# Kernel optimization log

Measured on AMD Instinct MI355X. Metric: run time of the kernel, lower is better.

Reference implementation:

```python
import jax, jax.numpy as jnp
import numpy as np

EPS = 1e-5

def _make_mask(rng, outdim, indim, expand_size, k=3):
    # Mirrors ExpanderConv2d mask construction (indim <= outdim branch when equal)
    m = np.zeros((outdim, indim), dtype=np.float32)
    if indim > outdim:
        for i in range(outdim):
            idx = rng.permutation(indim)[:expand_size]
            m[i, idx] = 1.0
    else:
        for i in range(indim):
            idx = rng.permutation(outdim)[:expand_size]
            m[idx, i] = 1.0
    return jnp.asarray(np.broadcast_to(m[:, :, None, None], (outdim, indim, k, k)).copy())

def _bn(x, gamma, beta, mean, var):
    # eval-mode BatchNorm2d over channel axis (NCHW)
    inv = gamma / jnp.sqrt(var + EPS)
    return x * inv[None, :, None, None] + (beta - mean * inv)[None, :, None, None]

def _conv3x3(x, w, stride=1):
    return jax.lax.conv_general_dilated(
        x, w, window_strides=(stride, stride), padding=((1, 1), (1, 1)),
        dimension_numbers=('NCHW', 'OIHW', 'NCHW'))

def setup_inputs() -> dict:
    key = jax.random.key(0)
    ks = jax.random.split(key, 4)
    C = 256
    x = jax.random.normal(ks[0], (64, C, 32, 32), dtype=jnp.float32)
    fan_out = C * 9
    std = float(np.sqrt(2.0 / fan_out))  # kaiming_normal_, mode='fan_out'
    w1 = jax.random.normal(ks[1], (C, C, 3, 3), dtype=jnp.float32) * std
    w2 = jax.random.normal(ks[2], (C, C, 3, 3), dtype=jnp.float32) * std
    rng = np.random.default_rng(0)
    mask1 = _make_mask(rng, C, C, C // 8)
    mask2 = _make_mask(rng, C, C, C // 8)
    g = jax.random.uniform(ks[3], (4 * C,), minval=0.5, maxval=1.5, dtype=jnp.float32)
    return {
        'x': x,
        'bn1_gamma': g[:C], 'bn1_beta': jnp.zeros((C,), jnp.float32),
        'bn1_mean': jnp.zeros((C,), jnp.float32), 'bn1_var': jnp.ones((C,), jnp.float32),
        'w1': w1, 'mask1': mask1,
        'bn2_gamma': g[C:2 * C], 'bn2_beta': jnp.zeros((C,), jnp.float32),
        'bn2_mean': jnp.zeros((C,), jnp.float32), 'bn2_var': jnp.ones((C,), jnp.float32),
        'w2': w2, 'mask2': mask2,
    }

def reference(x, bn1_gamma, bn1_beta, bn1_mean, bn1_var, w1, mask1,
              bn2_gamma, bn2_beta, bn2_mean, bn2_var, w2, mask2):
    out = jax.nn.relu(_bn(x, bn1_gamma, bn1_beta, bn1_mean, bn1_var))
    out = _conv3x3(out, w1 * mask1)          # masked expander conv, dropout(p=0)=identity
    out = jax.nn.relu(_bn(out, bn2_gamma, bn2_beta, bn2_mean, bn2_var))
    out = _conv3x3(out, w2 * mask2, stride=1)
    return out + x                            # identity shortcut (stride=1, in==out)
```

## Files before the change

kernel.cpp:

```cpp
#include <hip/hip_runtime.h>
#include <hip/hip_bf16.h>
#include <stdint.h>

typedef __bf16 bf16_t;
typedef __bf16 bf16x8 __attribute__((ext_vector_type(8)));
typedef __bf16 bf16x4 __attribute__((ext_vector_type(4)));
typedef float  f32x4  __attribute__((ext_vector_type(4)));

#define AS_GLOBAL __attribute__((address_space(1)))
#define AS_LDS    __attribute__((address_space(3)))

static constexpr int CCH   = 256;
static constexpr int HP    = 34;
static constexpr int PLANE = HP * HP;

__global__ void prep_params_k(const float* g1, const float* b1, const float* m1, const float* v1,
                              const float* g2, const float* b2, const float* m2, const float* v2,
                              float* prm) {
  int i = threadIdx.x;
  float i1 = g1[i] * rsqrtf(v1[i] + 1e-5f);
  prm[i]       = i1;
  prm[256 + i] = b1[i] - m1[i] * i1;
  float i2 = g2[i] * rsqrtf(v2[i] + 1e-5f);
  prm[512 + i] = i2;
  prm[768 + i] = b2[i] - m2[i] * i2;
}

__global__ __launch_bounds__(256) void prep_weights_k(const float* __restrict__ w,
                                                      const float* __restrict__ msk,
                                                      bf16_t* __restrict__ out) {
  int idx = blockIdx.x * 256 + threadIdx.x;
  const float* wp = w + (long)idx * 9;
  const float* mp = msk + (long)idx * 9;
#pragma unroll
  for (int khw = 0; khw < 9; ++khw)
    out[khw * 65536 + idx] = (bf16_t)(wp[khw] * mp[khw]);
}

__global__ __launch_bounds__(256) void zero_borders_k(bf16_t* __restrict__ t0p,
                                                      bf16_t* __restrict__ t1p) {
  const int bid = blockIdx.x;
  bf16_t* base = ((bid & 1) ? t1p : t0p) + (long)(bid >> 1) * PLANE * CCH;
  for (int i = threadIdx.x; i < 132 * 32; i += 256) {
    int pix = i >> 5, c16 = i & 31;
    int r, col;
    if (pix < 34)       { r = 0;           col = pix; }
    else if (pix < 68)  { r = 33;          col = pix - 34; }
    else if (pix < 100) { r = pix - 68 + 1; col = 0; }
    else                { r = pix - 100 + 1; col = 33; }
    *(f32x4*)&base[(r * HP + col) * CCH + c16 * 8] = f32x4{0.f, 0.f, 0.f, 0.f};
  }
}

__global__ __launch_bounds__(256) void prep_input_k(const float* __restrict__ x,
                                                    const float* __restrict__ prm,
                                                    bf16_t* __restrict__ t0p) {
  __shared__ __align__(16) bf16_t tile[64 * 256];
  const int tid = threadIdx.x;
  const int bid = blockIdx.x;
  const int n   = bid >> 4;
  const int p0  = (bid & 15) << 6;
  const int px    = tid & 63;
  const int cbase = tid >> 6;
  for (int r = 0; r < 64; ++r) {
    int ci = r * 4 + cbase;
    float v = x[((n * 256 + ci) << 10) + p0 + px];
    float y = fmaxf(v * prm[ci] + prm[256 + ci], 0.f);
    int byte = px * 512 + ((ci * 2) ^ ((px & 7) << 4));
    *(bf16_t*)((char*)tile + byte) = (bf16_t)y;
  }
  __syncthreads();
  for (int j = 0; j < 8; ++j) {
    int off  = j * 256 + tid;
    int pix  = off >> 5;
    int c16  = off & 31;
    int byte = pix * 512 + ((c16 * 16) ^ ((pix & 7) << 4));
    bf16x8 v = *(const bf16x8*)((char*)tile + byte);
    int p = p0 + pix;
    long gp = ((long)n * PLANE + ((p >> 5) + 1) * HP + (p & 31) + 1) * CCH + c16 * 8;
    *(bf16x8*)(t0p + gp) = v;
  }
}

template <int EPI>
__global__ __launch_bounds__(256, 2) void conv3x3_k(const bf16_t* __restrict__ inp,
                                                    const bf16_t* __restrict__ wts,
                                                    const float* __restrict__ prm,
                                                    const float* __restrict__ resid,
                                                    bf16_t* __restrict__ out_cl,
                                                    float* __restrict__ out_f) {
  __shared__ __align__(128) bf16_t As[2][4096];
  __shared__ __align__(128) bf16_t Bs[2][8192];

  const int tid  = threadIdx.x;
  const int lane = tid & 63;
  const int wid  = tid >> 6;
  const int wm   = wid >> 1;
  const int wn   = wid & 1;

  const int bid = blockIdx.x;
  const int w   = ((bid & 7) << 7) + (bid >> 3);
  const int co0 = (w & 1) << 7;
  const int pt  = w >> 1;
  const int n   = pt >> 3;
  const int hb  = (pt & 7) << 2;

  const int swz8 = (((lane & 3) ^ ((lane >> 2) & 3) ^ (lane >> 4)) << 3);
  const int l15  = lane & 15;

  f32x4 acc[4][4];
#pragma unroll
  for (int i = 0; i < 4; ++i)
#pragma unroll
    for (int j = 0; j < 4; ++j) acc[i][j] = f32x4{0.f, 0.f, 0.f, 0.f};

  auto stageA = [&](int ab, int c, int t) {
    const int ci0 = c << 5;
#pragma unroll
    for (int j = 0; j < 2; ++j) {
      const int ch  = wid * 2 + j;
      const int row = ch * 16 + (lane >> 2);
      const bf16_t* ga = wts + ((t * CCH + co0 + row) * CCH + ci0 + swz8);
      __builtin_amdgcn_global_load_lds((const AS_GLOBAL void*)ga,
                                       (AS_LDS void*)(&As[ab][ch * 512]), 16, 0, 0);
    }
  };

  auto stageB = [&](int bb, int c) {
    const int ci0 = c << 5;
#pragma unroll
    for (int j = 0; j < 4; ++j) {
      const int ibase = wid * 4 + j;
      int g = (ibase << 6) + lane;
      if (g > 815) g = 815;
      const int r  = g / 136;
      const int rm = g - r * 136;
      const bf16_t* gb = inp + ((n * PLANE + (hb + r) * HP + (rm >> 2)) * CCH + ci0 + ((rm & 3) << 3));
      __builtin_amdgcn_global_load_lds((const AS_GLOBAL void*)gb,
                                       (AS_LDS void*)(&Bs[bb][ibase * 512]), 16, 0, 0);
    }
  };

  stageB(0, 0);
  stageA(0, 0, 0);
  int ab = 0, bb = 0;
  for (int c = 0; c < 8; ++c) {
#pragma unroll
    for (int t = 0; t < 9; ++t) {
      __syncthreads();
      if (t < 8) stageA(ab ^ 1, c, t + 1);
      else if (c < 7) { stageB(bb ^ 1, c + 1); stageA(ab ^ 1, c + 1, 0); }
      const int kh = t / 3, kw = t - kh * 3;
      bf16x8 av[4], bv[4];
#pragma unroll
      for (int mi = 0; mi < 4; ++mi)
        av[mi] = *(const bf16x8*)&As[ab][((wm * 64 + mi * 16 + l15) << 5) + swz8];
#pragma unroll
      for (int ni = 0; ni < 4; ++ni) {
        const int p  = (wn << 6) + (ni << 4) + l15;
        const int pr = p >> 5, pc = p & 31;
        bv[ni] = *(const bf16x8*)&Bs[bb][((pr + kh) * 136 + (pc + kw) * 4 + (lane >> 4)) * 8];
      }
#pragma unroll
      for (int mi = 0; mi < 4; ++mi)
#pragma unroll
        for (int ni = 0; ni < 4; ++ni)
          acc[mi][ni] = __builtin_amdgcn_mfma_f32_16x16x32_bf16(av[mi], bv[ni], acc[mi][ni], 0, 0, 0);
      ab ^= 1;
    }
    bb ^= 1;
  }

  if (EPI == 0) {
#pragma unroll
    for (int mi = 0; mi < 4; ++mi) {
      const int co_b = co0 + wm * 64 + mi * 16 + ((lane >> 4) << 2);
      const float s0 = prm[co_b], s1 = prm[co_b + 1], s2 = prm[co_b + 2], s3 = prm[co_b + 3];
      const float t0 = prm[256 + co_b], t1 = prm[256 + co_b + 1],
                  t2 = prm[256 + co_b + 2], t3 = prm[256 + co_b + 3];
#pragma unroll
      for (int ni = 0; ni < 4; ++ni) {
        f32x4 v = acc[mi][ni];
        const int p  = (wn << 6) + (ni << 4) + l15;
        const int pr = p >> 5, pc = p & 31;
        bf16x4 pk;
        pk[0] = (bf16_t)fmaxf(v[0] * s0 + t0, 0.f);
        pk[1] = (bf16_t)fmaxf(v[1] * s1 + t1, 0.f);
        pk[2] = (bf16_t)fmaxf(v[2] * s2 + t2, 0.f);
        pk[3] = (bf16_t)fmaxf(v[3] * s3 + t3, 0.f);
        *(bf16x4*)&out_cl[(n * PLANE + (hb + pr + 1) * HP + pc + 1) * CCH + co_b] = pk;
      }
    }
  } else {
#pragma unroll
    for (int mi = 0; mi < 4; ++mi) {
      const int co_b = co0 + wm * 64 + mi * 16 + ((lane >> 4) << 2);
#pragma unroll
      for (int ni = 0; ni < 4; ++ni) {
        f32x4 v = acc[mi][ni];
        const int p  = (wn << 6) + (ni << 4) + l15;
        const int gp = ((n * CCH + co_b) << 10) + (hb << 5) + p;
        out_f[gp]        = v[0] + resid[gp];
        out_f[gp + 1024] = v[1] + resid[gp + 1024];
        out_f[gp + 2048] = v[2] + resid[gp + 2048];
        out_f[gp + 3072] = v[3] + resid[gp + 3072];
      }
    }
  }
}

extern "C" void kernel_launch(void* const* d_in, const int* in_sizes, int n_in,
                              void* d_out, int out_size, void* d_ws, size_t ws_size,
                              hipStream_t stream) {
  const float* x  = (const float*)d_in[0];
  const float* g1 = (const float*)d_in[1];
  const float* b1 = (const float*)d_in[2];
  const float* m1 = (const float*)d_in[3];
  const float* v1 = (const float*)d_in[4];
  const float* w1 = (const float*)d_in[5];
  const float* k1 = (const float*)d_in[6];
  const float* g2 = (const float*)d_in[7];
  const float* b2 = (const float*)d_in[8];
  const float* m2 = (const float*)d_in[9];
  const float* v2 = (const float*)d_in[10];
  const float* w2 = (const float*)d_in[11];
  const float* k2 = (const float*)d_in[12];

  char* ws = (char*)d_ws;
  const size_t T0P_B = (size_t)64 * PLANE * CCH * 2;
  bf16_t* t0p = (bf16_t*)ws;
  bf16_t* t1p = (bf16_t*)(ws + T0P_B);
  bf16_t* mw1 = (bf16_t*)(ws + 2 * T0P_B);
  bf16_t* mw2 = (bf16_t*)(ws + 2 * T0P_B + 1179648);
  float*  prm = (float*)(ws + 2 * T0P_B + 2 * 1179648);

  prep_params_k<<<1, 256, 0, stream>>>(g1, b1, m1, v1, g2, b2, m2, v2, prm);
  zero_borders_k<<<128, 256, 0, stream>>>(t0p, t1p);
  prep_weights_k<<<256, 256, 0, stream>>>(w1, k1, mw1);
  prep_weights_k<<<256, 256, 0, stream>>>(w2, k2, mw2);
  prep_input_k<<<1024, 256, 0, stream>>>(x, prm, t0p);

  conv3x3_k<0><<<1024, 256, 0, stream>>>(t0p, mw1, prm + 512, nullptr, t1p, nullptr);
  conv3x3_k<1><<<1024, 256, 0, stream>>>(t1p, mw2, nullptr, x, nullptr, (float*)d_out);
}
```

Baseline: 200.6 us.

## Restructure conv kernel with larger pixel tiles, 32x32 MFMA and register-prefetched weights

The implicit-GEMM conv kernel now covers 256 pixels (8 rows) per block instead of 128, halving the grid to 512 blocks. It switches from 16x16x32 to 32x32x16 bf16 MFMA with 16-wide accumulators. Weights are loaded straight from global memory into registers, double-buffered one tap ahead, so the LDS A buffer and most per-tap barriers go away. Input halo tiles are staged in LDS with one barrier per channel chunk and explicit vmcnt waits, and MFMA issue gets raised wave priority. In exchange, register pressure rises and fewer blocks are available to fill the CUs.

New measurement: 222.5 us. 1.11x slower.

```diff
diff --git a/kernel.cpp b/kernel.cpp
--- a/kernel.cpp
+++ b/kernel.cpp
@@ -6,9 +6,11 @@
 typedef __bf16 bf16x8 __attribute__((ext_vector_type(8)));
 typedef __bf16 bf16x4 __attribute__((ext_vector_type(4)));
 typedef float  f32x4  __attribute__((ext_vector_type(4)));
+typedef float  f32x16 __attribute__((ext_vector_type(16)));
 
 #define AS_GLOBAL __attribute__((address_space(1)))
 #define AS_LDS    __attribute__((address_space(3)))
+#define VMW(N) asm volatile("s_waitcnt vmcnt(" #N ")" ::: "memory")
 
 static constexpr int CCH   = 256;
 static constexpr int HP    = 34;
@@ -89,8 +91,7 @@
                                                     const float* __restrict__ resid,
                                                     bf16_t* __restrict__ out_cl,
                                                     float* __restrict__ out_f) {
-  __shared__ __align__(128) bf16_t As[2][4096];
-  __shared__ __align__(128) bf16_t Bs[2][8192];
+  __shared__ __align__(128) bf16_t Bs[2][12288];
 
   const int tid  = threadIdx.x;
   const int lane = tid & 63;
@@ -99,113 +100,144 @@
   const int wn   = wid & 1;
 
   const int bid = blockIdx.x;
-  const int w   = ((bid & 7) << 7) + (bid >> 3);
+  const int w   = ((bid & 7) << 6) + (bid >> 3);
   const int co0 = (w & 1) << 7;
   const int pt  = w >> 1;
-  const int n   = pt >> 3;
-  const int hb  = (pt & 7) << 2;
-
-  const int swz8 = (((lane & 3) ^ ((lane >> 2) & 3) ^ (lane >> 4)) << 3);
-  const int l15  = lane & 15;
-
-  f32x4 acc[4][4];
-#pragma unroll
-  for (int i = 0; i < 4; ++i)
-#pragma unroll
-    for (int j = 0; j < 4; ++j) acc[i][j] = f32x4{0.f, 0.f, 0.f, 0.f};
-
-  auto stageA = [&](int ab, int c, int t) {
-    const int ci0 = c << 5;
-#pragma unroll
-    for (int j = 0; j < 2; ++j) {
-      const int ch  = wid * 2 + j;
-      const int row = ch * 16 + (lane >> 2);
-      const bf16_t* ga = wts + ((t * CCH + co0 + row) * CCH + ci0 + swz8);
-      __builtin_amdgcn_global_load_lds((const AS_GLOBAL void*)ga,
-                                       (AS_LDS void*)(&As[ab][ch * 512]), 16, 0, 0);
-    }
-  };
-
-  auto stageB = [&](int bb, int c) {
-    const int ci0 = c << 5;
-#pragma unroll
-    for (int j = 0; j < 4; ++j) {
-      const int ibase = wid * 4 + j;
-      int g = (ibase << 6) + lane;
-      if (g > 815) g = 815;
-      const int r  = g / 136;
-      const int rm = g - r * 136;
-      const bf16_t* gb = inp + ((n * PLANE + (hb + r) * HP + (rm >> 2)) * CCH + ci0 + ((rm & 3) << 3));
-      __builtin_amdgcn_global_load_lds((const AS_GLOBAL void*)gb,
-                                       (AS_LDS void*)(&Bs[bb][ibase * 512]), 16, 0, 0);
-    }
-  };
-
-  stageB(0, 0);
-  stageA(0, 0, 0);
-  int ab = 0, bb = 0;
-  for (int c = 0; c < 8; ++c) {
-#pragma unroll
-    for (int t = 0; t < 9; ++t) {
-      __syncthreads();
-      if (t < 8) stageA(ab ^ 1, c, t + 1);
-      else if (c < 7) { stageB(bb ^ 1, c + 1); stageA(ab ^ 1, c + 1, 0); }
-      const int kh = t / 3, kw = t - kh * 3;
-      bf16x8 av[4], bv[4];
-#pragma unroll
-      for (int mi = 0; mi < 4; ++mi)
-        av[mi] = *(const bf16x8*)&As[ab][((wm * 64 + mi * 16 + l15) << 5) + swz8];
-#pragma unroll
-      for (int ni = 0; ni < 4; ++ni) {
-        const int p  = (wn << 6) + (ni << 4) + l15;
-        const int pr = p >> 5, pc = p & 31;
-        bv[ni] = *(const bf16x8*)&Bs[bb][((pr + kh) * 136 + (pc + kw) * 4 + (lane >> 4)) * 8];
+  const int n   = pt >> 2;
+  const int hb  = (pt & 3) << 3;
+
+  const int l31 = lane & 31;
+  const int k5  = lane >> 5;
+
+  const long aBase = (long)(co0 + wm * 64 + l31) * CCH + k5 * 8;
+  const int  bBase = k5 * 2720 + wn * 1088 + l31 * 8;
+
+  int bofs[6];
+#pragma unroll
+  for (int j = 0; j < 6; ++j) {
+    int idx = j * 256 + tid;
+    if (idx > 1359) idx = 1359;
+    const int g   = idx / 340;
+    const int rem = idx - g * 340;
+    const int r   = rem / 34;
+    const int cc  = rem - r * 34;
+    bofs[j] = (n * PLANE + (hb + r) * HP + cc) * CCH + g * 8;
+  }
+
+  f32x16 acc[2][4];
+#pragma unroll
+  for (int i = 0; i < 2; ++i)
+#pragma unroll
+    for (int j = 0; j < 4; ++j)
+#pragma unroll
+      for (int e = 0; e < 16; ++e) acc[i][j][e] = 0.f;
+
+  bf16x8 avA[4], avB[4], bv[8];
+
+#define STB(BBUF, CI0N, J) do {                                                      \
+    const bf16_t* gb_ = inp + bofs[J] + (CI0N);                                      \
+    __builtin_amdgcn_global_load_lds((const AS_GLOBAL void*)gb_,                     \
+        (AS_LDS void*)(&Bs[BBUF][((J) * 256 + tid) * 8]), 16, 0, 0);                 \
+  } while (0)
+
+#define APREF(SET, CI0N, TT) do {                                                    \
+    _Pragma("unroll") for (int mi = 0; mi < 2; ++mi)                                 \
+    _Pragma("unroll") for (int ks = 0; ks < 2; ++ks)                                 \
+      SET[mi * 2 + ks] = *(const bf16x8*)(wts + (long)(TT) * 65536 + aBase           \
+                                          + mi * 8192 + (CI0N) + ks * 16);           \
+  } while (0)
+
+#define MFMA16(SET) do {                                                             \
+    _Pragma("unroll") for (int mi = 0; mi < 2; ++mi)                                 \
+    _Pragma("unroll") for (int nj = 0; nj < 4; ++nj)                                 \
+    _Pragma("unroll") for (int ks = 0; ks < 2; ++ks)                                 \
+      acc[mi][nj] = __builtin_amdgcn_mfma_f32_32x32x16_bf16(                         \
+          SET[mi * 2 + ks], bv[nj * 2 + ks], acc[mi][nj], 0, 0, 0);                  \
+  } while (0)
+
+#define TAPB(T, PAR, LASTC) do {                                                     \
+    constexpr int KH = (T) / 3, KW = (T) % 3;                                        \
+    _Pragma("unroll") for (int nj = 0; nj < 4; ++nj)                                 \
+    _Pragma("unroll") for (int ks = 0; ks < 2; ++ks)                                 \
+      bv[nj * 2 + ks] = *(const bf16x8*)&bsrd[bBase + ks * 5440                      \
+                                              + (nj + KH) * 272 + KW * 8];           \
+    if (!(LASTC) && (T) <= 5) STB((c + 1) & 1, (c + 1) << 5, T);                     \
+    if (!((LASTC) && (T) == 8)) {                                                    \
+      constexpr int TN = ((T) + 1) % 9;                                              \
+      const int cin = ((T) == 8) ? ((c + 1) << 5) : (c << 5);                        \
+      if (((PAR) + (T)) & 1) { APREF(avA, cin, TN); } else { APREF(avB, cin, TN); }  \
+    }                                                                                \
+    __builtin_amdgcn_s_setprio(1);                                                   \
+    if (((PAR) + (T)) & 1) { MFMA16(avB); } else { MFMA16(avA); }                    \
+    __builtin_amdgcn_s_setprio(0);                                                   \
+  } while (0)
+
+#define CHUNKB(PAR, LASTC) do {                                                      \
+    const bf16_t* bsrd = &Bs[c & 1][0];                                              \
+    TAPB(0, PAR, LASTC); TAPB(1, PAR, LASTC); TAPB(2, PAR, LASTC);                   \
+    TAPB(3, PAR, LASTC); TAPB(4, PAR, LASTC); TAPB(5, PAR, LASTC);                   \
+    TAPB(6, PAR, LASTC); TAPB(7, PAR, LASTC); TAPB(8, PAR, LASTC);                   \
+    if (!(LASTC)) { VMW(0); __builtin_amdgcn_s_barrier(); }                          \
+  } while (0)
+
+  STB(0, 0, 0); STB(0, 0, 1); STB(0, 0, 2); STB(0, 0, 3); STB(0, 0, 4); STB(0, 0, 5);
+  APREF(avA, 0, 0);
+  VMW(0);
+  __builtin_amdgcn_s_barrier();
+
+  int c = 0;
+#pragma unroll 1
+  for (int it = 0; it < 3; ++it) {
+    CHUNKB(0, 0); ++c;
+    CHUNKB(1, 0); ++c;
+  }
+  CHUNKB(0, 0); ++c;
+  CHUNKB(1, 1);
+
+#undef TAPB
+#undef CHUNKB
+#undef APREF
+#undef MFMA16
+#undef STB
+
+  if (EPI == 0) {
+#pragma unroll
+    for (int mi = 0; mi < 2; ++mi)
+#pragma unroll
+      for (int nj = 0; nj < 4; ++nj) {
+        const int prow = hb + wn * 4 + nj;
+        const long pbase = ((long)n * PLANE + (prow + 1) * HP + l31 + 1) * CCH;
+#pragma unroll
+        for (int q = 0; q < 4; ++q) {
+          const int co_b = co0 + wm * 64 + mi * 32 + q * 8 + k5 * 4;
+          const float s0 = prm[co_b], s1 = prm[co_b + 1], s2 = prm[co_b + 2], s3 = prm[co_b + 3];
+          const float t0 = prm[256 + co_b], t1 = prm[256 + co_b + 1],
+                      t2 = prm[256 + co_b + 2], t3 = prm[256 + co_b + 3];
+          bf16x4 pk;
+          pk[0] = (bf16_t)fmaxf(acc[mi][nj][q * 4 + 0] * s0 + t0, 0.f);
+          pk[1] = (bf16_t)fmaxf(acc[mi][nj][q * 4 + 1] * s1 + t1, 0.f);
+          pk[2] = (bf16_t)fmaxf(acc[mi][nj][q * 4 + 2] * s2 + t2, 0.f);
+          pk[3] = (bf16_t)fmaxf(acc[mi][nj][q * 4 + 3] * s3 + t3, 0.f);
+          *(bf16x4*)&out_cl[pbase + co_b] = pk;
+        }
       }
-#pragma unroll
-      for (int mi = 0; mi < 4; ++mi)
-#pragma unroll
-        for (int ni = 0; ni < 4; ++ni)
-          acc[mi][ni] = __builtin_amdgcn_mfma_f32_16x16x32_bf16(av[mi], bv[ni], acc[mi][ni], 0, 0, 0);
-      ab ^= 1;
-    }
-    bb ^= 1;
-  }
-
-  if (EPI == 0) {
-#pragma unroll
-    for (int mi = 0; mi < 4; ++mi) {
-      const int co_b = co0 + wm * 64 + mi * 16 + ((lane >> 4) << 2);
-      const float s0 = prm[co_b], s1 = prm[co_b + 1], s2 = prm[co_b + 2], s3 = prm[co_b + 3];
-      const float t0 = prm[256 + co_b], t1 = prm[256 + co_b + 1],
-                  t2 = prm[256 + co_b + 2], t3 = prm[256 + co_b + 3];
-#pragma unroll
-      for (int ni = 0; ni < 4; ++ni) {
-        f32x4 v = acc[mi][ni];
-        const int p  = (wn << 6) + (ni << 4) + l15;
-        const int pr = p >> 5, pc = p & 31;
-        bf16x4 pk;
-        pk[0] = (bf16_t)fmaxf(v[0] * s0 + t0, 0.f);
-        pk[1] = (bf16_t)fmaxf(v[1] * s1 + t1, 0.f);
-        pk[2] = (bf16_t)fmaxf(v[2] * s2 + t2, 0.f);
-        pk[3] = (bf16_t)fmaxf(v[3] * s3 + t3, 0.f);
-        *(bf16x4*)&out_cl[(n * PLANE + (hb + pr + 1) * HP + pc + 1) * CCH + co_b] = pk;
+  } else {
+#pragma unroll
+    for (int mi = 0; mi < 2; ++mi)
+#pragma unroll
+      for (int nj = 0; nj < 4; ++nj) {
+        const int prow = hb + wn * 4 + nj;
+        const int ppos = prow * 32 + l31;
+#pragma unroll
+        for (int q = 0; q < 4; ++q) {
+          const int co_b = co0 + wm * 64 + mi * 32 + q * 8 + k5 * 4;
+#pragma unroll
+          for (int e = 0; e < 4; ++e) {
+            const long gp = (((long)n * CCH + co_b + e) << 10) + ppos;
+            out_f[gp] = acc[mi][nj][q * 4 + e] + resid[gp];
+          }
+        }
       }
-    }
-  } else {
-#pragma unroll
-    for (int mi = 0; mi < 4; ++mi) {
-      const int co_b = co0 + wm * 64 + mi * 16 + ((lane >> 4) << 2);
-#pragma unroll
-      for (int ni = 0; ni < 4; ++ni) {
-        f32x4 v = acc[mi][ni];
-        const int p  = (wn << 6) + (ni << 4) + l15;
-        const int gp = ((n * CCH + co_b) << 10) + (hb << 5) + p;
-        out_f[gp]        = v[0] + resid[gp];
-        out_f[gp + 1024] = v[1] + resid[gp + 1024];
-        out_f[gp + 2048] = v[2] + resid[gp + 2048];
-        out_f[gp + 3072] = v[3] + resid[gp + 3072];
-      }
-    }
   }
 }
 
@@ -240,6 +272,6 @@
   prep_weights_k<<<256, 256, 0, stream>>>(w2, k2, mw2);
   prep_input_k<<<1024, 256, 0, stream>>>(x, prm, t0p);
 
-  conv3x3_k<0><<<1024, 256, 0, stream>>>(t0p, mw1, prm + 512, nullptr, t1p, nullptr);
-  conv3x3_k<1><<<1024, 256, 0, stream>>>(t1p, mw2, nullptr, x, nullptr, (float*)d_out);
-}
+  conv3x3_k<0><<<512, 256, 0, stream>>>(t0p, mw1, prm + 512, nullptr, t1p, nullptr);
+  conv3x3_k<1><<<512, 256, 0, stream>>>(t1p, mw2, nullptr, x, nullptr, (float*)d_out);
+}
```
